# Performance work log

Measured on AMD Instinct MI355X. Metric: run time of the kernel, lower is better.

## Reference

```python
import jax, jax.numpy as jnp
import numpy as np

N_X_AXIS = 128
N_Y_AXIS = 128
X_RANGE = (-2.0, 2.0)
Y_RANGE = (-2.0, 2.0)
BATCH = 4
N_CTX = 1024


def make_grid():
    # Give_2d_Grid: flattened (n_x*n_y, 2) grid, x-major (consistent with
    # the view(batch, n_x_axis, n_y_axis, 3) reshape in forward).
    gx = jnp.linspace(X_RANGE[0], X_RANGE[1], N_X_AXIS, dtype=jnp.float32)
    gy = jnp.linspace(Y_RANGE[0], Y_RANGE[1], N_Y_AXIS, dtype=jnp.float32)
    xx, yy = jnp.meshgrid(gx, gy, indexing='ij')  # (n_x, n_y)
    return jnp.stack([xx.ravel(), yy.ravel()], axis=-1)  # (n_x*n_y, 2)


def setup_inputs() -> dict:
    key = jax.random.key(0)
    k1, k2 = jax.random.split(key)
    X = jax.random.normal(k1, (BATCH, N_CTX, 2), dtype=jnp.float32)
    Y = jax.random.normal(k2, (BATCH, N_CTX, 2), dtype=jnp.float32)
    grid = make_grid()
    return {"X": X, "Y": Y, "grid": grid}


def reference(X, Y, grid):
    # RBF Gram matrix between grid points and context points X.
    # k(a,b) = exp(-||a-b||^2 / (2 l^2)), l = 1 (default length scale).
    # d2: (B, G, n)
    d2 = jnp.sum((grid[None, :, None, :] - X[:, None, :, :]) ** 2, axis=-1)
    Gram = jnp.exp(-0.5 * d2)  # (B, G, n)

    # Psi: prepend a column of ones -> (B, n, 3)
    ones = jnp.ones(Y.shape[:2] + (1,), dtype=Y.dtype)
    Expand_Y = jnp.concatenate([ones, Y], axis=-1)

    # Feature map: (B, G, 3)
    FM = jnp.einsum('bgn,bnc->bgc', Gram, Expand_Y)

    # Density-normalize the value channels by the density channel.
    density = FM[..., 0:1]
    FM = jnp.concatenate([density, FM[..., 1:] / density], axis=-1)

    # (B, G, 3) -> (B, n_x, n_y, 3) -> (B, 3, n_y, n_x)
    out = FM.reshape(X.shape[0], N_X_AXIS, N_Y_AXIS, 3)
    return out.transpose(0, 3, 2, 1)
```

## Files before the change

kernel.cpp:

```cpp
#include <hip/hip_runtime.h>


#define N_CTX   1024
#define G_PER_B 16384
#define NQ      64
#define CHUNK   (N_CTX / NQ)
#define TPB     4
#define SSTRIDE (CHUNK + 1)

typedef float fv4 __attribute__((ext_vector_type(4)));

__device__ __forceinline__ float fast_exp2(float x) {
#if __has_builtin(__builtin_amdgcn_exp2f)
  return __builtin_amdgcn_exp2f(x);
#else
  return exp2f(x);
#endif
}

#define RED_BYTES (32 * TPB * 13 * 16)
#define S_BYTES   ((N_CTX + NQ) * 16)

__global__ __launch_bounds__(256, 4) void convcnp_encoder_kernel(
    const float* __restrict__ X,
    const float* __restrict__ Y,
    const float* __restrict__ grid,
    float* __restrict__ out)
{
  __shared__ __attribute__((aligned(16))) unsigned char smem[RED_BYTES];
  float4* s = (float4*)smem;
  fv4 (*red)[TPB][13] = (fv4 (*)[TPB][13])smem;

  const int t    = threadIdx.x;
  const int tile = t & (TPB - 1);
  const int q    = t >> 2;

  const int tau = blockIdx.x * TPB + tile;
  const int b   = tau >> 10;
  const int rem = tau & 1023;
  const int ixt = rem & 31;
  const int jyt = rem >> 5;

  const float SC = 0.84932180028801907f;

  const float2* Xb = (const float2*)(X + b * (N_CTX * 2));
  const float2* Yb = (const float2*)(Y + b * (N_CTX * 2));
#pragma unroll
  for (int k = 0; k < 4; ++k) {
    int n = t + 256 * k;
    float2 x = Xb[n];
    float2 y = Yb[n];
    s[n + (n >> 4)] = make_float4(x.x * SC, x.y * SC, y.x, y.y);
  }

  fv4 gxs;
#pragma unroll
  for (int a = 0; a < 4; ++a)
    gxs[a] = grid[(4 * ixt + a) * 256] * SC;
  float gys[4];
#pragma unroll
  for (int bb = 0; bb < 4; ++bb)
    gys[bb] = grid[2 * (4 * jyt + bb) + 1] * SC;

  __syncthreads();

  fv4 acc0[4], acc1[4], acc2[4];
#pragma unroll
  for (int bb = 0; bb < 4; ++bb) {
    acc0[bb] = (fv4){0.f, 0.f, 0.f, 0.f};
    acc1[bb] = (fv4){0.f, 0.f, 0.f, 0.f};
    acc2[bb] = (fv4){0.f, 0.f, 0.f, 0.f};
  }

  const float4* sp = &s[q * SSTRIDE];
#pragma unroll 4
  for (int it = 0; it < CHUNK; ++it) {
    float4 v = sp[it];
    fv4 dx = gxs - v.x;
    fv4 ex;
#pragma unroll
    for (int a = 0; a < 4; ++a) ex[a] = fast_exp2(-(dx[a] * dx[a]));
    float ey[4], ey0[4], ey1[4];
#pragma unroll
    for (int bb = 0; bb < 4; ++bb) {
      float dy = gys[bb] - v.y;
      float e  = fast_exp2(-(dy * dy));
      ey[bb]  = e;
      ey0[bb] = e * v.z;
      ey1[bb] = e * v.w;
    }
#pragma unroll
    for (int bb = 0; bb < 4; ++bb) {
      acc0[bb] += ex * ey[bb];
      acc1[bb] += ex * ey0[bb];
      acc2[bb] += ex * ey1[bb];
    }
  }

  __syncthreads();

#pragma unroll
  for (int step = 32; step >= 1; step >>= 1) {
    if (q >= step && q < 2 * step) {
      fv4* d = &red[q - step][tile][0];
#pragma unroll
      for (int bb = 0; bb < 4; ++bb) {
        d[bb] = acc0[bb]; d[4 + bb] = acc1[bb]; d[8 + bb] = acc2[bb];
      }
    }
    __syncthreads();
    if (q < step) {
      fv4* r = &red[q][tile][0];
#pragma unroll
      for (int bb = 0; bb < 4; ++bb) {
        acc0[bb] += r[bb]; acc1[bb] += r[4 + bb]; acc2[bb] += r[8 + bb];
      }
    }
    __syncthreads();
  }

  if (q == 0) {
    const int ob = b * (3 * G_PER_B) + jyt * 4 * 128 + ixt * 4;
#pragma unroll
    for (int bb = 0; bb < 4; ++bb) {
      fv4 d  = acc0[bb];
      fv4 o1 = acc1[bb] / d;
      fv4 o2 = acc2[bb] / d;
      const int row = ob + bb * 128;
      *(fv4*)(out + row)                = d;
      *(fv4*)(out + row + G_PER_B)      = o1;
      *(fv4*)(out + row + 2 * G_PER_B)  = o2;
    }
  }
}

extern "C" void kernel_launch(void* const* d_in, const int* in_sizes, int n_in,
                              void* d_out, int out_size, void* d_ws, size_t ws_size,
                              hipStream_t stream) {
  const float* X    = (const float*)d_in[0];
  const float* Y    = (const float*)d_in[1];
  const float* grid = (const float*)d_in[2];
  float* out        = (float*)d_out;

  convcnp_encoder_kernel<<<dim3(1024), dim3(256), 0, stream>>>(X, Y, grid, out);
}
```

Measured before the change: 71.66 us.

## Precompute separable RBF exp tables in a prologue kernel and stream them in main loop

Splits the work into two kernels. The first builds per-context-point exp tables for the x and y grid axes, with the y table also pre-weighted by Y, and writes them to workspace. The main kernel then loads these tables from global memory instead of recomputing exp2 for each grid tile. This removes redundant transcendental work repeated across tiles. In exchange it writes and reads about 8 MB of workspace, adds a second launch, and drops the LDS staging of inputs.

```diff
diff --git a/kernel.cpp b/kernel.cpp
--- a/kernel.cpp
+++ b/kernel.cpp
@@ -6,7 +6,7 @@
 #define NQ      64
 #define CHUNK   (N_CTX / NQ)
 #define TPB     4
-#define SSTRIDE (CHUNK + 1)
+#define PLANE   (4 * 1024 * 128)
 
 typedef float fv4 __attribute__((ext_vector_type(4)));
 
@@ -18,18 +18,47 @@
 #endif
 }
 
-#define RED_BYTES (32 * TPB * 13 * 16)
-#define S_BYTES   ((N_CTX + NQ) * 16)
-
-__global__ __launch_bounds__(256, 4) void convcnp_encoder_kernel(
+__global__ __launch_bounds__(256) void build_tables_kernel(
     const float* __restrict__ X,
     const float* __restrict__ Y,
     const float* __restrict__ grid,
+    float* __restrict__ W)
+{
+  const float SC = 0.84932180028801907f;
+  const int tid = blockIdx.x * 256 + threadIdx.x;
+  const int p = tid >> 5;
+  const int c = tid & 31;
+
+  const float2 x = ((const float2*)X)[p];
+  const float2 y = ((const float2*)Y)[p];
+
+  fv4 ex, ey, ey0, ey1;
+#pragma unroll
+  for (int a = 0; a < 4; ++a) {
+    const int i = c * 4 + a;
+    const float gx = grid[i * 256];
+    const float gy = grid[2 * i + 1];
+    const float dx = SC * (gx - x.x);
+    ex[a] = fast_exp2(-(dx * dx));
+    const float dy = SC * (gy - x.y);
+    const float e  = fast_exp2(-(dy * dy));
+    ey[a]  = e;
+    ey0[a] = e * y.x;
+    ey1[a] = e * y.y;
+  }
+
+  const int base = p * 128 + c * 4;
+  *(fv4*)(W + base)             = ex;
+  *(fv4*)(W + PLANE + base)     = ey;
+  *(fv4*)(W + 2 * PLANE + base) = ey0;
+  *(fv4*)(W + 3 * PLANE + base) = ey1;
+}
+
+__global__ __launch_bounds__(256, 4) void convcnp_main_kernel(
+    const float* __restrict__ W,
     float* __restrict__ out)
 {
-  __shared__ __attribute__((aligned(16))) unsigned char smem[RED_BYTES];
-  float4* s = (float4*)smem;
-  fv4 (*red)[TPB][13] = (fv4 (*)[TPB][13])smem;
+  __shared__ fv4 red[NQ / 2][TPB][13];
 
   const int t    = threadIdx.x;
   const int tile = t & (TPB - 1);
@@ -41,28 +70,11 @@
   const int ixt = rem & 31;
   const int jyt = rem >> 5;
 
-  const float SC = 0.84932180028801907f;
-
-  const float2* Xb = (const float2*)(X + b * (N_CTX * 2));
-  const float2* Yb = (const float2*)(Y + b * (N_CTX * 2));
-#pragma unroll
-  for (int k = 0; k < 4; ++k) {
-    int n = t + 256 * k;
-    float2 x = Xb[n];
-    float2 y = Yb[n];
-    s[n + (n >> 4)] = make_float4(x.x * SC, x.y * SC, y.x, y.y);
-  }
-
-  fv4 gxs;
-#pragma unroll
-  for (int a = 0; a < 4; ++a)
-    gxs[a] = grid[(4 * ixt + a) * 256] * SC;
-  float gys[4];
-#pragma unroll
-  for (int bb = 0; bb < 4; ++bb)
-    gys[bb] = grid[2 * (4 * jyt + bb) + 1] * SC;
-
-  __syncthreads();
+  const int nrow = b * (N_CTX * 128) + q * (CHUNK * 128);
+  const float* pEx  = W + nrow + 4 * ixt;
+  const float* pEy  = W + PLANE + nrow + 4 * jyt;
+  const float* pEy0 = pEy + PLANE;
+  const float* pEy1 = pEy + 2 * PLANE;
 
   fv4 acc0[4], acc1[4], acc2[4];
 #pragma unroll
@@ -72,32 +84,20 @@
     acc2[bb] = (fv4){0.f, 0.f, 0.f, 0.f};
   }
 
-  const float4* sp = &s[q * SSTRIDE];
 #pragma unroll 4
   for (int it = 0; it < CHUNK; ++it) {
-    float4 v = sp[it];
-    fv4 dx = gxs - v.x;
-    fv4 ex;
-#pragma unroll
-    for (int a = 0; a < 4; ++a) ex[a] = fast_exp2(-(dx[a] * dx[a]));
-    float ey[4], ey0[4], ey1[4];
-#pragma unroll
-    for (int bb = 0; bb < 4; ++bb) {
-      float dy = gys[bb] - v.y;
-      float e  = fast_exp2(-(dy * dy));
-      ey[bb]  = e;
-      ey0[bb] = e * v.z;
-      ey1[bb] = e * v.w;
-    }
+    const int o = it * 128;
+    fv4 ex = *(const fv4*)(pEx + o);
+    fv4 ey = *(const fv4*)(pEy + o);
+    fv4 e0 = *(const fv4*)(pEy0 + o);
+    fv4 e1 = *(const fv4*)(pEy1 + o);
 #pragma unroll
     for (int bb = 0; bb < 4; ++bb) {
       acc0[bb] += ex * ey[bb];
-      acc1[bb] += ex * ey0[bb];
-      acc2[bb] += ex * ey1[bb];
+      acc1[bb] += ex * e0[bb];
+      acc2[bb] += ex * e1[bb];
     }
   }
-
-  __syncthreads();
 
 #pragma unroll
   for (int step = 32; step >= 1; step >>= 1) {
@@ -141,6 +141,8 @@
   const float* Y    = (const float*)d_in[1];
   const float* grid = (const float*)d_in[2];
   float* out        = (float*)d_out;
+  float* W          = (float*)d_ws;
 
-  convcnp_encoder_kernel<<<dim3(1024), dim3(256), 0, stream>>>(X, Y, grid, out);
+  build_tables_kernel<<<dim3(512), dim3(256), 0, stream>>>(X, Y, grid, W);
+  convcnp_main_kernel<<<dim3(1024), dim3(256), 0, stream>>>(W, out);
 }
```

After: 89.52 us. 24.9% more time.
